# Kernel tuning notes

Hardware: AMD Instinct MI355X
Metric: run time of the kernel (lower is better)

Reference implementation:

```python
import jax, jax.numpy as jnp
import numpy as np

E, IN, H, OUT = 8, 512, 1024, 512   # num_experts, input_size, hidden_size, output_size
HH = H // 2                          # expert-MLP hidden (512)
GIN, GH = 5, E                       # gating GRU input / hidden


def gru_layer(x, w_ih, w_hh, b_ih, b_hh):
    """torch.nn.GRU single layer, batch_first. x: [B,T,I] -> ys: [B,T,Hd].
    Gate order in 3*Hd dims: reset, update, new."""
    Hd = w_hh.shape[1]
    def step(h, xt):
        gi = xt @ w_ih.T + b_ih          # [B,3Hd]
        gh = h @ w_hh.T + b_hh
        ir, iz, inn = jnp.split(gi, 3, axis=-1)
        hr, hz, hn = jnp.split(gh, 3, axis=-1)
        r = jax.nn.sigmoid(ir + hr)
        z = jax.nn.sigmoid(iz + hz)
        n = jnp.tanh(inn + r * hn)
        h = (1.0 - z) * n + z * h
        return h, h
    h0 = jnp.zeros((x.shape[0], Hd), x.dtype)
    _, ys = jax.lax.scan(step, h0, jnp.swapaxes(x, 0, 1))
    return jnp.swapaxes(ys, 0, 1)


def _uniform(key, shape, fan_in, fan_out):
    bound = np.sqrt(6.0 / (fan_in * fan_out))
    return jax.random.uniform(key, shape, jnp.float32, -bound, bound)


def setup_inputs() -> dict:
    key = jax.random.key(0)
    ks = jax.random.split(key, 16)
    g = 1.0 / np.sqrt(GH)
    m = 1.0 / np.sqrt(H)
    inp = {
        "X": jax.random.normal(ks[0], (128, 100, IN), jnp.float32),
        # gating GRU: 2 layers, input 5 -> hidden E
        "gw_ih0": jax.random.uniform(ks[1], (3 * GH, GIN), jnp.float32, -g, g),
        "gw_hh0": jax.random.uniform(ks[2], (3 * GH, GH), jnp.float32, -g, g),
        "gb_ih0": jnp.zeros((3 * GH,), jnp.float32),
        "gb_hh0": jnp.zeros((3 * GH,), jnp.float32),
        "gw_ih1": jax.random.uniform(ks[3], (3 * GH, GH), jnp.float32, -g, g),
        "gw_hh1": jax.random.uniform(ks[4], (3 * GH, GH), jnp.float32, -g, g),
        "gb_ih1": jnp.zeros((3 * GH,), jnp.float32),
        "gb_hh1": jnp.zeros((3 * GH,), jnp.float32),
        # main GRU: 1 layer, input IN -> hidden H
        "mw_ih": jax.random.uniform(ks[5], (3 * H, IN), jnp.float32, -m, m),
        "mw_hh": jax.random.uniform(ks[6], (3 * H, H), jnp.float32, -m, m),
        "mb_ih": jnp.zeros((3 * H,), jnp.float32),
        "mb_hh": jnp.zeros((3 * H,), jnp.float32),
        # expert MLP weights [E, in, out], biases [E, out]
        "w1": _uniform(ks[7], (E, H, HH), H, HH),
        "b1": jnp.zeros((E, HH), jnp.float32),
        "w2": _uniform(ks[8], (E, HH, HH), HH, HH),
        "b2": jnp.zeros((E, HH), jnp.float32),
        "w3": _uniform(ks[9], (E, HH, OUT), HH, OUT),
        "b3": jnp.zeros((E, OUT), jnp.float32),
    }
    return inp


def _moe_layer(x, coef, w, b):
    # same math as sum(x[...,None] * sum_e(coef_e * W_e), dim=1) + coef @ b
    return jnp.einsum("be,bi,eio->bo", coef, x, w) + coef @ b


def reference(X, gw_ih0, gw_hh0, gb_ih0, gb_hh0, gw_ih1, gw_hh1, gb_ih1, gb_hh1,
              mw_ih, mw_hh, mb_ih, mb_hh, w1, b1, w2, b2, w3, b3):
    Xg = X[:, :, -GIN:]
    h0 = gru_layer(Xg, gw_ih0, gw_hh0, gb_ih0, gb_hh0)
    h1 = gru_layer(h0, gw_ih1, gw_hh1, gb_ih1, gb_hh1)
    omega = jax.nn.softmax(h1[:, -1, :], axis=-1)          # [B,E]
    Z = gru_layer(X, mw_ih, mw_hh, mb_ih, mb_hh)[:, -1, :]  # [B,H]
    a1 = jax.nn.elu(_moe_layer(Z, omega, w1, b1))
    a2 = jax.nn.elu(_moe_layer(a1, omega, w2, b2))
    Y = _moe_layer(a2, omega, w3, b3)
    return jnp.clip(Y, 0.0, 1.0)
```

## Files before the change

kernel.cpp:

```cpp
#include <hip/hip_runtime.h>
#include <cmath>

#define B_   128
#define T_   100
#define IN_  512
#define H_   1024
#define E_   8
#define HH_  512
#define GIN_ 5
#define GH_  8

#define A_LO_  49152
#define BOFF_  98304
#define LDSZ2  147456
#define A_LOF 49152
#define BB_HI 98304
#define BB_LO 114688
#define LDSZF 131072

typedef unsigned long long u64t;
typedef unsigned int uint32;
typedef __attribute__((ext_vector_type(8))) short bf16x8;
typedef __attribute__((ext_vector_type(4))) float f32x4;

__device__ __forceinline__ float sigf(float x) { return 1.0f / (1.0f + expf(-x)); }

__device__ __forceinline__ float4 ld_h4_sc1(const float4* p) {
  const u64t* q = (const u64t*)p;
  u64t a = __hip_atomic_load(q,     __ATOMIC_RELAXED, __HIP_MEMORY_SCOPE_AGENT);
  u64t b = __hip_atomic_load(q + 1, __ATOMIC_RELAXED, __HIP_MEMORY_SCOPE_AGENT);
  union { u64t u; float2 f; } ca, cb;
  ca.u = a; cb.u = b;
  return make_float4(ca.f.x, ca.f.y, cb.f.x, cb.f.y);
}

__device__ __forceinline__ void st_u64_sc1(void* p, u64t v) {
  __hip_atomic_store((u64t*)p, v, __ATOMIC_RELAXED, __HIP_MEMORY_SCOPE_AGENT);
}

__device__ __forceinline__ void gridbar(unsigned* c) {
  __syncthreads();
  if (threadIdx.x == 0) {
    __hip_atomic_fetch_add(c, 1u, __ATOMIC_RELEASE, __HIP_MEMORY_SCOPE_AGENT);
    while (__hip_atomic_load(c, __ATOMIC_RELAXED, __HIP_MEMORY_SCOPE_AGENT) < gridDim.x) {
      __builtin_amdgcn_s_sleep(1);
    }
  }
  __syncthreads();
}

__device__ __forceinline__ uint32 bf16_rne(float f) {
  uint32 u = __builtin_bit_cast(uint32, f);
  return (u + 0x7FFFu + ((u >> 16) & 1u)) >> 16;
}

__device__ __forceinline__ void split2(float f0, float f1, uint32& h, uint32& l) {
  uint32 h0 = bf16_rne(f0), h1 = bf16_rne(f1);
  float hf0 = __builtin_bit_cast(float, h0 << 16);
  float hf1 = __builtin_bit_cast(float, h1 << 16);
  uint32 l0 = bf16_rne(f0 - hf0), l1 = bf16_rne(f1 - hf1);
  h = h0 | (h1 << 16);
  l = l0 | (l1 << 16);
}

__device__ __forceinline__ void gl_lds16(const char* g, char* l) {
  __builtin_amdgcn_global_load_lds(
      (const __attribute__((address_space(1))) uint32*)(const void*)g,
      (__attribute__((address_space(3))) uint32*)(void*)l, 16, 0, 0);
}

__global__ __launch_bounds__(256) void xsplit_kernel(
    const float* __restrict__ X, char* __restrict__ xpl)
{
  int idx = blockIdx.x * 256 + threadIdx.x;
  int lane = idx & 63;
  int n   = (idx >> 6) & 7;
  int KT  = (idx >> 9) & 15;
  int t   = idx >> 13;
  int b   = n * 16 + (lane & 15);
  int k   = KT * 32 + ((lane >> 4) << 3);
  const float* src = X + ((size_t)b * T_ + t) * IN_ + k;
  float4 va = *(const float4*)src;
  float4 vb = *(const float4*)(src + 4);
  uint32 h0,h1,h2,h3,l0,l1,l2,l3;
  split2(va.x, va.y, h0, l0); split2(va.z, va.w, h1, l1);
  split2(vb.x, vb.y, h2, l2); split2(vb.z, vb.w, h3, l3);
  size_t off = ((((size_t)t * 16 + KT) * 8 + n) << 10) + ((size_t)lane << 4);
  *(uint4*)(xpl + off)            = make_uint4(h0, h1, h2, h3);
  *(uint4*)(xpl + 13107200 + off) = make_uint4(l0, l1, l2, l3);
}

__global__ __launch_bounds__(1024, 4) void gru_mfma2(
    const char* __restrict__ xpl, char* __restrict__ ringp,
    const float* __restrict__ wih, const float* __restrict__ whh,
    const float* __restrict__ bih, const float* __restrict__ bhh,
    float* __restrict__ hq, unsigned* __restrict__ barr)
{
  extern __shared__ char lds[];
  const int tid  = threadIdx.x;
  const int lane = tid & 63;
  const int wv   = __builtin_amdgcn_readfirstlane(tid >> 6);
  const int nt   = wv & 7;
  const int ktw  = wv >> 3;
  const int j0   = blockIdx.x << 2;

  for (int ii = tid * 2; ii < 24576; ii += 2048) {
    int r = ii / 1536, k = ii - r * 1536;
    int jj = r & 3, g = r >> 2;
    float f0, f1;
    if (k < IN_) {
      if (g == 3) { f0 = 0.f; f1 = 0.f; }
      else {
        const float* p = wih + (size_t)(((g == 2 ? 2 : g) * H_) + j0 + jj) * IN_ + k;
        f0 = p[0]; f1 = p[1];
      }
    } else {
      if (g == 2) { f0 = 0.f; f1 = 0.f; }
      else {
        const float* p = whh + (size_t)(((g == 3 ? 2 : g) * H_) + j0 + jj) * H_ + (k - IN_);
        f0 = p[0]; f1 = p[1];
      }
    }
    uint32 h, l; split2(f0, f1, h, l);
    int KT = k >> 5, k32 = k & 31;
    int ln  = r + ((k32 >> 3) << 4);
    int off = (KT << 10) + (ln << 4) + ((k32 & 7) << 1);
    *(uint32*)(lds + off)         = h;
    *(uint32*)(lds + A_LO_ + off) = l;
  }

  const int ejj = tid >> 7, eb = tid & 127;
  float bir = 0.f, biz = 0.f, bin = 0.f, bhr = 0.f, bhz = 0.f, bhn = 0.f;
  if (tid < 512) {
    int j = j0 + ejj;
    bir = bih[j]; biz = bih[H_ + j]; bin = bih[2 * H_ + j];
    bhr = bhh[j]; bhz = bhh[H_ + j]; bhn = bhh[2 * H_ + j];
  }
  float hprev_r = 0.f;
  __syncthreads();

  const char* xsrc0 = xpl + (size_t)ktw * 13107200 + ((size_t)nt << 10) + ((size_t)lane << 4);
  const char* hsrc0 = ringp + (size_t)ktw * 262144 + ((size_t)nt << 10) + ((size_t)lane << 4);
  char* const tilebase = lds + BOFF_ + (((ktw << 3) + nt) << 10);

  const size_t pw_off = ((((size_t)(j0 >> 5)) * 8) << 10);

  for (int t = 0; t < T_; ++t) {
    const char* xs = xsrc0 + (size_t)t * 131072;
    const char* hs = hsrc0 + (size_t)t * 524288;
    f32x4 acc = {0.f, 0.f, 0.f, 0.f};

#define STAGE(cc) { const char* g = ((cc) < 16) ? (xs + (size_t)(cc) * 8192) \
                                                : (hs + (size_t)((cc) - 16) * 8192); \
                    gl_lds16(g, lds + BOFF_ + ((cc) % 3) * 16384 - BOFF_ + BOFF_ \
                             + (((ktw << 3) + nt) << 10) - (((ktw << 3) + nt) << 10) \
                             + ((cc) % 3) * 0); }
#undef STAGE

    gl_lds16(xs + 0 * 8192, tilebase + 0 * 16384);
    gl_lds16(xs + 1 * 8192, tilebase + 1 * 16384);

    #pragma unroll
    for (int c = 0; c < 48; ++c) {
      if (c < 46) {
        const int cn = c + 2;
        const char* g = (cn < 16) ? (xs + (size_t)cn * 8192)
                                  : (hs + (size_t)(cn - 16) * 8192);
        gl_lds16(g, tilebase + (cn % 3) * 16384);
        asm volatile("s_waitcnt vmcnt(2)" ::: "memory");
      } else if (c == 46) {
        asm volatile("s_waitcnt vmcnt(1)" ::: "memory");
      } else {
        asm volatile("s_waitcnt vmcnt(0)" ::: "memory");
      }
      __builtin_amdgcn_s_barrier();
      __builtin_amdgcn_sched_barrier(0);
      if (ktw == (c & 1)) {
        bf16x8 ah = *(const bf16x8*)(lds + (c << 10) + (lane << 4));
        bf16x8 al = *(const bf16x8*)(lds + A_LO_ + (c << 10) + (lane << 4));
        const char* bb = lds + BOFF_ + (c % 3) * 16384;
        bf16x8 bh = *(const bf16x8*)(bb + (nt << 10) + (lane << 4));
        bf16x8 bl = *(const bf16x8*)(bb + 8192 + (nt << 10) + (lane << 4));
        acc = __builtin_amdgcn_mfma_f32_16x16x32_bf16(ah, bh, acc, 0, 0, 0);
        acc = __builtin_amdgcn_mfma_f32_16x16x32_bf16(ah, bl, acc, 0, 0, 0);
        acc = __builtin_amdgcn_mfma_f32_16x16x32_bf16(al, bh, acc, 0, 0, 0);
      }
      __builtin_amdgcn_sched_barrier(0);
      __builtin_amdgcn_s_barrier();
    }

    *(f32x4*)(lds + BOFF_ + (((ktw << 3) + nt) << 10) + (lane << 4)) = acc;
    __syncthreads();

    if (tid < 512) {
      float sv[4];
      #pragma unroll
      for (int g = 0; g < 4; ++g) {
        int lr = (eb & 15) | (g << 4);
        const char* d0 = lds + BOFF_ + (((eb >> 4)) << 10) + (lr << 4) + (ejj << 2);
        float v0 = *(const float*)d0;
        float v1 = *(const float*)(d0 + 8192);
        sv[g] = v0 + v1;
      }
      float rr = sigf(sv[0] + bir + bhr);
      float zz = sigf(sv[1] + biz + bhz);
      float nn = tanhf(sv[2] + bin + rr * (sv[3] + bhn));
      float hv = (1.f - zz) * nn + zz * hprev_r;
      hprev_r = hv;
      ((float*)(lds + BOFF_ + 16384))[(ejj << 7) + eb] = hv;
      if (t == T_ - 1) hq[((blockIdx.x * 128 + eb) << 2) + ejj] = hv;
    }
    __syncthreads();

    if (tid < 128) {
      const int b = tid;
      const float* hl = (const float*)(lds + BOFF_ + 16384);
      uint32 hh[4], ll[4];
      #pragma unroll
      for (int i = 0; i < 4; ++i) {
        float v = hl[(i << 7) + b];
        uint32 hb = bf16_rne(v);
        float hf = __builtin_bit_cast(float, hb << 16);
        ll[i] = bf16_rne(v - hf);
        hh[i] = hb;
      }
      u64t HI = (u64t)hh[0] | ((u64t)hh[1] << 16) | ((u64t)hh[2] << 32) | ((u64t)hh[3] << 48);
      u64t LO = (u64t)ll[0] | ((u64t)ll[1] << 16) | ((u64t)ll[2] << 32) | ((u64t)ll[3] << 48);
      int lane_w = (((j0 & 31) >> 3) << 4) | (b & 15);
      size_t byteoff = pw_off + (((size_t)(b >> 4)) << 10) + ((size_t)lane_w << 4) + ((j0 & 4) ? 8 : 0);
      char* base = ringp + (size_t)(t + 1) * 524288;
      st_u64_sc1(base + byteoff, HI);
      st_u64_sc1(base + 262144 + byteoff, LO);
    }
    gridbar(barr + t);
  }
}

__device__ __forceinline__ int boff(int kt, int nt, int lane) {
  return (((((kt << 3) + nt) << 6) + lane) << 4) ^ ((nt & 3) << 5);
}

__global__ __launch_bounds__(256) void xt_kernel(
    const float* __restrict__ X, float4* __restrict__ XT4)
{
  int idx = blockIdx.x * 256 + threadIdx.x;
  int b  = idx & 127;
  int kq = (idx >> 7) & 127;
  int t  = idx >> 14;
  XT4[idx] = *(const float4*)(X + ((size_t)b * T_ + t) * IN_ + kq * 4);
}

template<bool RING>
__global__ __launch_bounds__(1024, 4) void gru_mfma(
    const float4* __restrict__ XT4, const float* __restrict__ X, int use_xt,
    const float* __restrict__ wih, const float* __restrict__ whh,
    const float* __restrict__ bih, const float* __restrict__ bhh,
    float* __restrict__ ring, unsigned* __restrict__ barr)
{
  extern __shared__ char lds[];
  const int tid  = threadIdx.x;
  const int lane = tid & 63;
  const int wv   = __builtin_amdgcn_readfirstlane(tid >> 6);
  const int nt   = wv & 7;
  const int ktw  = wv >> 3;
  const int j0   = blockIdx.x << 2;

  for (int ii = tid * 2; ii < 24576; ii += 2048) {
    int r = ii / 1536, k = ii - r * 1536;
    int jj = r & 3, g = r >> 2;
    float f0, f1;
    if (k < IN_) {
      if (g == 3) { f0 = 0.f; f1 = 0.f; }
      else {
        const float* p = wih + (size_t)(((g == 2 ? 2 : g) * H_) + j0 + jj) * IN_ + k;
        f0 = p[0]; f1 = p[1];
      }
    } else {
      if (g == 2) { f0 = 0.f; f1 = 0.f; }
      else {
        const float* p = whh + (size_t)(((g == 3 ? 2 : g) * H_) + j0 + jj) * H_ + (k - IN_);
        f0 = p[0]; f1 = p[1];
      }
    }
    uint32 h, l; split2(f0, f1, h, l);
    int KT = k >> 5, k32 = k & 31;
    int ln  = r + ((k32 >> 3) << 4);
    int off = (KT << 10) + (ln << 4) + ((k32 & 7) << 1);
    *(uint32*)(lds + off)         = h;
    *(uint32*)(lds + A_LOF + off) = l;
  }

  const int ejj = tid >> 7, eb = tid & 127;
  float bir = 0.f, biz = 0.f, bin = 0.f, bhr = 0.f, bhz = 0.f, bhn = 0.f;
  if (tid < 512) {
    int j = j0 + ejj;
    bir = bih[j]; biz = bih[H_ + j]; bin = bih[2 * H_ + j];
    bhr = bhh[j]; bhz = bhh[H_ + j]; bhn = bhh[2 * H_ + j];
  }
  __syncthreads();

  const int kq_loc = tid >> 7;
  const int sb     = tid & 127;
  const int s_nt   = sb >> 4;
  const int lane_w = (sb & 15) + ((kq_loc >> 1) << 4);
  const int sub8   = (kq_loc & 1) << 3;

  for (int t = 0; t < T_; ++t) {
    const float4* __restrict__ hp4 =
        (const float4*)ring + (size_t)(RING ? t : (t & 1)) * 32768;
    float* __restrict__ hnf =
        ring + (size_t)(RING ? (t + 1) : ((t + 1) & 1)) * 131072;
    const float4* __restrict__ xt_t = XT4 + (size_t)t * 16384;

    f32x4 acc = {0.f, 0.f, 0.f, 0.f};

    #pragma unroll 1
    for (int c = 0; c < 24; ++c) {
      #pragma unroll
      for (int i = 0; i < 2; ++i) {
        int kqg = (c << 4) + kq_loc + (i << 3);
        float4 v;
        if (kqg < 128) {
          if (use_xt) v = xt_t[kqg * 128 + sb];
          else        v = *(const float4*)(X + ((size_t)sb * T_ + t) * IN_ + (kqg << 2));
        } else {
          v = RING ? hp4[(kqg - 128) * 128 + sb]
                   : ld_h4_sc1(hp4 + (kqg - 128) * 128 + sb);
        }
        uint32 h01, h23, l01, l23;
        split2(v.x, v.y, h01, l01);
        split2(v.z, v.w, h23, l23);
        int bo = boff(i, s_nt, lane_w) + sub8;
        *(uint2*)(lds + BB_HI + bo) = make_uint2(h01, h23);
        *(uint2*)(lds + BB_LO + bo) = make_uint2(l01, l23);
      }
      __syncthreads();
      {
        int KT = (c << 1) + ktw;
        bf16x8 ah = *(const bf16x8*)(lds + (KT << 10) + (lane << 4));
        bf16x8 al = *(const bf16x8*)(lds + A_LOF + (KT << 10) + (lane << 4));
        int bo = boff(ktw, nt, lane);
        bf16x8 bh = *(const bf16x8*)(lds + BB_HI + bo);
        bf16x8 bl = *(const bf16x8*)(lds + BB_LO + bo);
        acc = __builtin_amdgcn_mfma_f32_16x16x32_bf16(ah, bh, acc, 0, 0, 0);
        acc = __builtin_amdgcn_mfma_f32_16x16x32_bf16(ah, bl, acc, 0, 0, 0);
        acc = __builtin_amdgcn_mfma_f32_16x16x32_bf16(al, bh, acc, 0, 0, 0);
      }
      __syncthreads();
    }

    *(f32x4*)(lds + BB_HI + boff(ktw, nt, lane)) = acc;
    __syncthreads();
    if (tid < 512) {
      float sv[4];
      #pragma unroll
      for (int g = 0; g < 4; ++g) {
        int r  = (g << 2) + ejj;
        int lr = (eb & 15) + ((r >> 2) << 4);
        int rg = (r & 3) << 2;
        float v0 = *(const float*)(lds + BB_HI + boff(0, eb >> 4, lr) + rg);
        float v1 = *(const float*)(lds + BB_HI + boff(1, eb >> 4, lr) + rg);
        sv[g] = v0 + v1;
      }
      float rr = sigf(sv[0] + bir + bhr);
      float zz = sigf(sv[1] + biz + bhz);
      float nn = tanhf(sv[2] + bin + rr * (sv[3] + bhn));
      int hidx = ((blockIdx.x * 128 + eb) << 2) + ejj;
      float hpv;
      if (RING) hpv = ((const float*)hp4)[hidx];
      else      hpv = __hip_atomic_load(&((const float*)hp4)[hidx],
                                        __ATOMIC_RELAXED, __HIP_MEMORY_SCOPE_AGENT);
      float hv = (1.f - zz) * nn + zz * hpv;
      __hip_atomic_store(&hnf[hidx], hv, __ATOMIC_RELAXED, __HIP_MEMORY_SCOPE_AGENT);
    }
    gridbar(barr + t);
  }
}

__global__ __launch_bounds__(256) void hfin_kernel(
    const float* __restrict__ h4, float* __restrict__ out)
{
  int idx = blockIdx.x * 256 + threadIdx.x;
  int b = idx >> 10, k = idx & 1023;
  out[idx] = h4[(((k >> 2) * 128 + b) << 2) + (k & 3)];
}

__global__ __launch_bounds__(64, 1) void gating_kernel(
    const float* __restrict__ X,
    const float* __restrict__ gwih0, const float* __restrict__ gwhh0,
    const float* __restrict__ gbih0, const float* __restrict__ gbhh0,
    const float* __restrict__ gwih1, const float* __restrict__ gwhh1,
    const float* __restrict__ gbih1, const float* __restrict__ gbhh1,
    float* __restrict__ omega)
{
  const int b = blockIdx.x;
  const int g = threadIdx.x;
  const int u = g & 7;
  float wi0[GIN_] = {}, wh0[GH_] = {}, wi1[GH_] = {}, wh1[GH_] = {};
  float bi0 = 0.f, bh0 = 0.f, bi1 = 0.f, bh1 = 0.f;
  if (g < 3 * GH_) {
    #pragma unroll
    for (int i = 0; i < GIN_; ++i) wi0[i] = gwih0[g * GIN_ + i];
    #pragma unroll
    for (int k = 0; k < GH_; ++k) { wh0[k] = gwhh0[g * GH_ + k]; wi1[k] = gwih1[g * GH_ + k]; wh1[k] = gwhh1[g * GH_ + k]; }
    bi0 = gbih0[g]; bh0 = gbhh0[g]; bi1 = gbih1[g]; bh1 = gbhh1[g];
  }
  float h0[GH_] = {}, h1[GH_] = {};
  for (int t = 0; t < T_; ++t) {
    float xt[GIN_];
    #pragma unroll
    for (int i = 0; i < GIN_; ++i) xt[i] = X[((size_t)b * T_ + t) * IN_ + (IN_ - GIN_) + i];
    float px = bi0, ph = bh0;
    #pragma unroll
    for (int i = 0; i < GIN_; ++i) px = fmaf(xt[i], wi0[i], px);
    #pragma unroll
    for (int k = 0; k < GH_; ++k) ph = fmaf(h0[k], wh0[k], ph);
    float s = px + ph;
    float s_r = __shfl(s, u);
    float s_z = __shfl(s, 8 + u);
    float nval = tanhf(px + sigf(s_r) * ph);
    float zval = sigf(s_z);
    float hnew = (1.f - zval) * nval + zval * h0[u];
    #pragma unroll
    for (int k = 0; k < GH_; ++k) h0[k] = __shfl(hnew, 16 + k);
    float px1 = bi1, ph1 = bh1;
    #pragma unroll
    for (int k = 0; k < GH_; ++k) px1 = fmaf(h0[k], wi1[k], px1);
    #pragma unroll
    for (int k = 0; k < GH_; ++k) ph1 = fmaf(h1[k], wh1[k], ph1);
    float s1 = px1 + ph1;
    float s1r = __shfl(s1, u);
    float s1z = __shfl(s1, 8 + u);
    float n1 = tanhf(px1 + sigf(s1r) * ph1);
    float z1 = sigf(s1z);
    float h1new = (1.f - z1) * n1 + z1 * h1[u];
    #pragma unroll
    for (int k = 0; k < GH_; ++k) h1[k] = __shfl(h1new, 16 + k);
  }
  if (g < GH_) {
    float m = h1[0];
    #pragma unroll
    for (int k = 1; k < GH_; ++k) m = fmaxf(m, h1[k]);
    float sum = 0.f;
    #pragma unroll
    for (int k = 0; k < GH_; ++k) sum += expf(h1[k] - m);
    omega[b * GH_ + g] = expf(h1[g] - m) / sum;
  }
}

__global__ __launch_bounds__(256, 2) void moe_kernel(
    const float* __restrict__ in, const float* __restrict__ w,
    const float* __restrict__ bias, const float* __restrict__ omega,
    float* __restrict__ out, int K, int act)
{
  __shared__ float4 lin4[64 * 32];
  __shared__ float  ldsw[E_ * 4 * 128];
  const int tid  = threadIdx.x;
  const int bh   = blockIdx.x & 1;
  const int jt   = blockIdx.x >> 1;
  const int wv   = tid >> 6;
  const int lane = tid & 63;
  const int j0   = jt * 4;
  const int j    = __builtin_amdgcn_readfirstlane(j0 + wv);
  const int b    = bh * 64 + lane;

  float acc[E_] = {0.f,0.f,0.f,0.f,0.f,0.f,0.f,0.f};
  const float4* row4 = &lin4[lane * 32];
  const int nch = K / 128;

  for (int c = 0; c < nch; ++c) {
    __syncthreads();
    const int k0 = c * 128;
    #pragma unroll
    for (int it = 0; it < 8; ++it) {
      int f = it * 256 + tid;
      int bb = f >> 5, q = f & 31;
      float4 v = *(const float4*)(in + (size_t)(bh * 64 + bb) * K + k0 + q * 4);
      lin4[bb * 32 + ((q & 24) | ((q ^ bb) & 7))] = v;
    }
    #pragma unroll
    for (int it = 0; it < 4; ++it) {
      int f = it * 256 + tid;
      int e = f >> 7, k = f & 127;
      float4 v = *(const float4*)(w + ((size_t)e * K + k0 + k) * HH_ + j0);
      ldsw[(e * 4 + 0) * 128 + k] = v.x;
      ldsw[(e * 4 + 1) * 128 + k] = v.y;
      ldsw[(e * 4 + 2) * 128 + k] = v.z;
      ldsw[(e * 4 + 3) * 128 + k] = v.w;
    }
    __syncthreads();
    #pragma unroll 2
    for (int q = 0; q < 32; ++q) {
      float4 xv = row4[(q & 24) | ((q ^ lane) & 7)];
      #pragma unroll
      for (int e = 0; e < E_; ++e) {
        const float4 wq = *(const float4*)&ldsw[(e * 4 + wv) * 128 + 4 * q];
        acc[e] = fmaf(xv.x, wq.x, acc[e]);
        acc[e] = fmaf(xv.y, wq.y, acc[e]);
        acc[e] = fmaf(xv.z, wq.z, acc[e]);
        acc[e] = fmaf(xv.w, wq.w, acc[e]);
      }
    }
  }

  float om[E_];
  #pragma unroll
  for (int e = 0; e < E_; ++e) om[e] = omega[b * E_ + e];
  float v = 0.f;
  #pragma unroll
  for (int e = 0; e < E_; ++e) v = fmaf(om[e], acc[e] + bias[e * HH_ + j], v);
  if (act == 0) v = (v > 0.f) ? v : expm1f(v);
  else          v = fminf(fmaxf(v, 0.f), 1.f);
  out[(size_t)b * HH_ + j] = v;
}

extern "C" void kernel_launch(void* const* d_in, const int* in_sizes, int n_in,
                              void* d_out, int out_size, void* d_ws, size_t ws_size,
                              hipStream_t stream) {
  (void)in_sizes; (void)n_in; (void)out_size;
  const float* X     = (const float*)d_in[0];
  const float* gwih0 = (const float*)d_in[1];
  const float* gwhh0 = (const float*)d_in[2];
  const float* gbih0 = (const float*)d_in[3];
  const float* gbhh0 = (const float*)d_in[4];
  const float* gwih1 = (const float*)d_in[5];
  const float* gwhh1 = (const float*)d_in[6];
  const float* gbih1 = (const float*)d_in[7];
  const float* gbhh1 = (const float*)d_in[8];
  const float* mwih  = (const float*)d_in[9];
  const float* mwhh  = (const float*)d_in[10];
  const float* mbih  = (const float*)d_in[11];
  const float* mbhh  = (const float*)d_in[12];
  const float* w1    = (const float*)d_in[13];
  const float* b1    = (const float*)d_in[14];
  const float* w2    = (const float*)d_in[15];
  const float* b2    = (const float*)d_in[16];
  const float* w3    = (const float*)d_in[17];
  const float* b3    = (const float*)d_in[18];

  const size_t HBUF = (size_t)B_ * H_;
  size_t tierS_f = 256 + HBUF + 101 * HBUF + 1024 + 2 * (size_t)B_ * HH_ + HBUF + 6553600;
  const size_t XTF = (size_t)T_ * IN_ * B_;
  size_t ringA = 256 + (size_t)(T_ + 1) * HBUF + HBUF + 1024 + 2 * (size_t)B_ * HH_ + XTF;
  size_t ringB = 256 + 2 * HBUF + HBUF + 1024 + 2 * (size_t)B_ * HH_ + XTF;

  float* ws = (float*)d_ws;

  if (ws_size >= tierS_f * sizeof(float)) {
    unsigned* barr = (unsigned*)ws;
    float* hq    = ws + 256;
    float* ringp = hq + HBUF;
    float* om    = ringp + 101 * HBUF;
    float* a1    = om + 1024;
    float* a2    = a1 + (size_t)B_ * HH_;
    float* hfin  = a2 + (size_t)B_ * HH_;
    float* xpl   = hfin + HBUF;

    (void)hipMemsetAsync(d_ws, 0, 256 * sizeof(float), stream);
    (void)hipMemsetAsync(ringp, 0, 524288, stream);
    (void)hipFuncSetAttribute((const void*)gru_mfma2,
                        hipFuncAttributeMaxDynamicSharedMemorySize, LDSZ2);

    gating_kernel<<<128, 64, 0, stream>>>(X, gwih0, gwhh0, gbih0, gbhh0,
                                          gwih1, gwhh1, gbih1, gbhh1, om);
    xsplit_kernel<<<3200, 256, 0, stream>>>(X, (char*)xpl);
    gru_mfma2<<<256, 1024, LDSZ2, stream>>>((const char*)xpl, (char*)ringp,
        mwih, mwhh, mbih, mbhh, hq, barr);
    hfin_kernel<<<512, 256, 0, stream>>>(hq, hfin);
    moe_kernel<<<256, 256, 0, stream>>>(hfin, w1, b1, om, a1, H_, 0);
    moe_kernel<<<256, 256, 0, stream>>>(a1, w2, b2, om, a2, HH_, 0);
    moe_kernel<<<256, 256, 0, stream>>>(a2, w3, b3, om, (float*)d_out, HH_, 1);
    return;
  }

  int tierA   = ws_size >= ringA * sizeof(float);
  int use_xt  = tierA || (ws_size >= ringB * sizeof(float));
  int R       = tierA ? (T_ + 1) : 2;

  unsigned* barr = (unsigned*)ws;
  float* ring = ws + 256;
  float* hfin = ring + (size_t)R * HBUF;
  float* om   = hfin + HBUF;
  float* a1   = om + 1024;
  float* a2   = a1 + (size_t)B_ * HH_;
  float* XT   = a2 + (size_t)B_ * HH_;

  (void)hipMemsetAsync(d_ws, 0, (256 + HBUF) * sizeof(float), stream);
  (void)hipFuncSetAttribute((const void*)gru_mfma<true>,
                      hipFuncAttributeMaxDynamicSharedMemorySize, LDSZF);
  (void)hipFuncSetAttribute((const void*)gru_mfma<false>,
                      hipFuncAttributeMaxDynamicSharedMemorySize, LDSZF);

  gating_kernel<<<128, 64, 0, stream>>>(X, gwih0, gwhh0, gbih0, gbhh0,
                                        gwih1, gwhh1, gbih1, gbhh1, om);
  if (use_xt)
    xt_kernel<<<(T_ * 128 * 128) / 256, 256, 0, stream>>>(X, (float4*)XT);

  if (tierA)
    gru_mfma<true><<<256, 1024, LDSZF, stream>>>((const float4*)XT, X, use_xt,
        mwih, mwhh, mbih, mbhh, ring, barr);
  else
    gru_mfma<false><<<256, 1024, LDSZF, stream>>>((const float4*)XT, X, use_xt,
        mwih, mwhh, mbih, mbhh, ring, barr);

  const float* hlast = ring + (size_t)(tierA ? T_ : (T_ & 1)) * HBUF;
  hfin_kernel<<<512, 256, 0, stream>>>(hlast, hfin);
  moe_kernel<<<256, 256, 0, stream>>>(hfin, w1, b1, om, a1, H_, 0);
  moe_kernel<<<256, 256, 0, stream>>>(a1, w2, b2, om, a2, HH_, 0);
  moe_kernel<<<256, 256, 0, stream>>>(a2, w3, b3, om, (float*)d_out, HH_, 1);
}
```

Before: 1.758 ms.

## Restructure GRU MFMA loop: paired K-chunks, register-held weights, cross-step prefetch

The persistent GRU kernel now computes two K-chunks per iteration, one per half of the waves, instead of leaving half the waves idle each chunk. This halves the number of barrier-separated iterations. The last 8 K-chunks of the recurrent weights are held in registers, which frees LDS for a double-buffered B staging area. The first x-chunk of the next timestep is prefetched before the step's reduction. The aim is to cut per-step barrier count and serial latency in the latency-bound recurrence, at the cost of more registers and more complex indexing under a 1024-thread, 4-wave-per-SIMD launch bound.

```diff
diff --git a/kernel.cpp b/kernel.cpp
--- a/kernel.cpp
+++ b/kernel.cpp
@@ -10,9 +10,10 @@
 #define GIN_ 5
 #define GH_  8
 
-#define A_LO_  49152
-#define BOFF_  98304
-#define LDSZ2  147456
+#define A_LO_  40960
+#define BOFF_  81920
+#define BOFF2_ 114688
+#define LDSZ4  147456
 #define A_LOF 49152
 #define BB_HI 98304
 #define BB_LO 114688
@@ -90,7 +91,27 @@
   *(uint4*)(xpl + 13107200 + off) = make_uint4(l0, l1, l2, l3);
 }
 
-__global__ __launch_bounds__(1024, 4) void gru_mfma2(
+__device__ __forceinline__ void stage_pair(
+    char* lds, const char* xpl, const char* ringp,
+    int q, int tx, int th, int sp, int spl, int snp, int lane)
+{
+  const int cc = 2 * q + sp;
+  char* dst0 = lds + BOFF_ + ((q & 1) << 15) + (sp << 14) + (spl << 13);
+  #pragma unroll
+  for (int i = 0; i < 2; ++i) {
+    const int nt = (snp << 1) + i;
+    const char* src;
+    if (cc < 16)
+      src = xpl + (size_t)spl * 13107200
+          + ((((size_t)tx * 16 + cc) * 8 + nt) << 10) + ((size_t)lane << 4);
+    else
+      src = ringp + (size_t)th * 524288 + ((size_t)spl << 18)
+          + ((size_t)((cc - 16) * 8 + nt) << 10) + ((size_t)lane << 4);
+    gl_lds16(src, dst0 + (nt << 10));
+  }
+}
+
+__global__ __launch_bounds__(1024, 4) void gru_mfma4(
     const char* __restrict__ xpl, char* __restrict__ ringp,
     const float* __restrict__ wih, const float* __restrict__ whh,
     const float* __restrict__ bih, const float* __restrict__ bhh,
@@ -100,12 +121,15 @@
   const int tid  = threadIdx.x;
   const int lane = tid & 63;
   const int wv   = __builtin_amdgcn_readfirstlane(tid >> 6);
-  const int nt   = wv & 7;
-  const int ktw  = wv >> 3;
+  const int cw   = wv >> 3;
+  const int ntc  = wv & 7;
+  const int sp   = wv & 1;
+  const int spl  = (wv >> 1) & 1;
+  const int snp  = wv >> 2;
   const int j0   = blockIdx.x << 2;
 
-  for (int ii = tid * 2; ii < 24576; ii += 2048) {
-    int r = ii / 1536, k = ii - r * 1536;
+  for (int ii = tid * 2; ii < 20480; ii += 2048) {
+    int r = ii / 1280, k = ii - r * 1280;
     int jj = r & 3, g = r >> 2;
     float f0, f1;
     if (k < IN_) {
@@ -129,6 +153,33 @@
     *(uint32*)(lds + A_LO_ + off) = l;
   }
 
+  bf16x8 rah[4], ral[4];
+  {
+    const int rr = lane & 15, k8 = lane >> 4;
+    const int jj = rr & 3, g = rr >> 2;
+    #pragma unroll
+    for (int i = 0; i < 4; ++i) {
+      const int KT = 40 + 2 * i + cw;
+      const int kh = KT * 32 + k8 * 8 - IN_;
+      bf16x8 hv, lv;
+      if (g == 2) {
+        #pragma unroll
+        for (int e = 0; e < 8; ++e) { hv[e] = 0; lv[e] = 0; }
+      } else {
+        const float* p = whh + (size_t)(((g == 3 ? 2 : g) * H_) + j0 + jj) * H_ + kh;
+        #pragma unroll
+        for (int e = 0; e < 8; ++e) {
+          float v = p[e];
+          uint32 hb = bf16_rne(v);
+          float hf = __builtin_bit_cast(float, hb << 16);
+          uint32 lb = bf16_rne(v - hf);
+          hv[e] = (short)hb; lv[e] = (short)lb;
+        }
+      }
+      rah[i] = hv; ral[i] = lv;
+    }
+  }
+
   const int ejj = tid >> 7, eb = tid & 127;
   float bir = 0.f, biz = 0.f, bin = 0.f, bhr = 0.f, bhz = 0.f, bhn = 0.f;
   if (tid < 512) {
@@ -137,50 +188,27 @@
     bhr = bhh[j]; bhz = bhh[H_ + j]; bhn = bhh[2 * H_ + j];
   }
   float hprev_r = 0.f;
+  const size_t pw_off = ((((size_t)(j0 >> 5)) * 8) << 10);
   __syncthreads();
 
-  const char* xsrc0 = xpl + (size_t)ktw * 13107200 + ((size_t)nt << 10) + ((size_t)lane << 4);
-  const char* hsrc0 = ringp + (size_t)ktw * 262144 + ((size_t)nt << 10) + ((size_t)lane << 4);
-  char* const tilebase = lds + BOFF_ + (((ktw << 3) + nt) << 10);
-
-  const size_t pw_off = ((((size_t)(j0 >> 5)) * 8) << 10);
+  stage_pair(lds, xpl, ringp, 0, 0, 0, sp, spl, snp, lane);
 
   for (int t = 0; t < T_; ++t) {
-    const char* xs = xsrc0 + (size_t)t * 131072;
-    const char* hs = hsrc0 + (size_t)t * 524288;
     f32x4 acc = {0.f, 0.f, 0.f, 0.f};
 
-#define STAGE(cc) { const char* g = ((cc) < 16) ? (xs + (size_t)(cc) * 8192) \
-                                                : (hs + (size_t)((cc) - 16) * 8192); \
-                    gl_lds16(g, lds + BOFF_ + ((cc) % 3) * 16384 - BOFF_ + BOFF_ \
-                             + (((ktw << 3) + nt) << 10) - (((ktw << 3) + nt) << 10) \
-                             + ((cc) % 3) * 0); }
-#undef STAGE
-
-    gl_lds16(xs + 0 * 8192, tilebase + 0 * 16384);
-    gl_lds16(xs + 1 * 8192, tilebase + 1 * 16384);
-
-    #pragma unroll
-    for (int c = 0; c < 48; ++c) {
-      if (c < 46) {
-        const int cn = c + 2;
-        const char* g = (cn < 16) ? (xs + (size_t)cn * 8192)
-                                  : (hs + (size_t)(cn - 16) * 8192);
-        gl_lds16(g, tilebase + (cn % 3) * 16384);
-        asm volatile("s_waitcnt vmcnt(2)" ::: "memory");
-      } else if (c == 46) {
-        asm volatile("s_waitcnt vmcnt(1)" ::: "memory");
-      } else {
-        asm volatile("s_waitcnt vmcnt(0)" ::: "memory");
-      }
+    #pragma unroll 4
+    for (int p = 0; p < 20; ++p) {
+      stage_pair(lds, xpl, ringp, p + 1, t, t, sp, spl, snp, lane);
+      asm volatile("s_waitcnt vmcnt(2)" ::: "memory");
       __builtin_amdgcn_s_barrier();
       __builtin_amdgcn_sched_barrier(0);
-      if (ktw == (c & 1)) {
+      {
+        const int c = 2 * p + cw;
         bf16x8 ah = *(const bf16x8*)(lds + (c << 10) + (lane << 4));
         bf16x8 al = *(const bf16x8*)(lds + A_LO_ + (c << 10) + (lane << 4));
-        const char* bb = lds + BOFF_ + (c % 3) * 16384;
-        bf16x8 bh = *(const bf16x8*)(bb + (nt << 10) + (lane << 4));
-        bf16x8 bl = *(const bf16x8*)(bb + 8192 + (nt << 10) + (lane << 4));
+        const char* bb = lds + BOFF_ + ((p & 1) << 15) + (cw << 14);
+        bf16x8 bh = *(const bf16x8*)(bb + (ntc << 10) + (lane << 4));
+        bf16x8 bl = *(const bf16x8*)(bb + 8192 + (ntc << 10) + (lane << 4));
         acc = __builtin_amdgcn_mfma_f32_16x16x32_bf16(ah, bh, acc, 0, 0, 0);
         acc = __builtin_amdgcn_mfma_f32_16x16x32_bf16(ah, bl, acc, 0, 0, 0);
         acc = __builtin_amdgcn_mfma_f32_16x16x32_bf16(al, bh, acc, 0, 0, 0);
@@ -189,7 +217,33 @@
       __builtin_amdgcn_s_barrier();
     }
 
-    *(f32x4*)(lds + BOFF_ + (((ktw << 3) + nt) << 10) + (lane << 4)) = acc;
+    #pragma unroll
+    for (int i = 0; i < 4; ++i) {
+      const int p = 20 + i;
+      if (p < 23) {
+        stage_pair(lds, xpl, ringp, p + 1, t, t, sp, spl, snp, lane);
+        asm volatile("s_waitcnt vmcnt(2)" ::: "memory");
+      } else if (t < T_ - 1) {
+        stage_pair(lds, xpl, ringp, 0, t + 1, t + 1, sp, spl, snp, lane);
+        asm volatile("s_waitcnt vmcnt(2)" ::: "memory");
+      } else {
+        asm volatile("s_waitcnt vmcnt(0)" ::: "memory");
+      }
+      __builtin_amdgcn_s_barrier();
+      __builtin_amdgcn_sched_barrier(0);
+      {
+        const char* bb = lds + BOFF_ + ((p & 1) << 15) + (cw << 14);
+        bf16x8 bh = *(const bf16x8*)(bb + (ntc << 10) + (lane << 4));
+        bf16x8 bl = *(const bf16x8*)(bb + 8192 + (ntc << 10) + (lane << 4));
+        acc = __builtin_amdgcn_mfma_f32_16x16x32_bf16(rah[i], bh, acc, 0, 0, 0);
+        acc = __builtin_amdgcn_mfma_f32_16x16x32_bf16(rah[i], bl, acc, 0, 0, 0);
+        acc = __builtin_amdgcn_mfma_f32_16x16x32_bf16(ral[i], bh, acc, 0, 0, 0);
+      }
+      __builtin_amdgcn_sched_barrier(0);
+      __builtin_amdgcn_s_barrier();
+    }
+
+    *(f32x4*)(lds + BOFF2_ + (((cw << 3) + ntc) << 10) + (lane << 4)) = acc;
     __syncthreads();
 
     if (tid < 512) {
@@ -197,7 +251,7 @@
       #pragma unroll
       for (int g = 0; g < 4; ++g) {
         int lr = (eb & 15) | (g << 4);
-        const char* d0 = lds + BOFF_ + (((eb >> 4)) << 10) + (lr << 4) + (ejj << 2);
+        const char* d0 = lds + BOFF2_ + (((eb >> 4)) << 10) + (lr << 4) + (ejj << 2);
         float v0 = *(const float*)d0;
         float v1 = *(const float*)(d0 + 8192);
         sv[g] = v0 + v1;
@@ -207,14 +261,14 @@
       float nn = tanhf(sv[2] + bin + rr * (sv[3] + bhn));
       float hv = (1.f - zz) * nn + zz * hprev_r;
       hprev_r = hv;
-      ((float*)(lds + BOFF_ + 16384))[(ejj << 7) + eb] = hv;
+      ((float*)(lds + BOFF2_ + 16384))[(ejj << 7) + eb] = hv;
       if (t == T_ - 1) hq[((blockIdx.x * 128 + eb) << 2) + ejj] = hv;
     }
     __syncthreads();
 
     if (tid < 128) {
       const int b = tid;
-      const float* hl = (const float*)(lds + BOFF_ + 16384);
+      const float* hl = (const float*)(lds + BOFF2_ + 16384);
       uint32 hh[4], ll[4];
       #pragma unroll
       for (int i = 0; i < 4; ++i) {
@@ -558,13 +612,13 @@
 
     (void)hipMemsetAsync(d_ws, 0, 256 * sizeof(float), stream);
     (void)hipMemsetAsync(ringp, 0, 524288, stream);
-    (void)hipFuncSetAttribute((const void*)gru_mfma2,
-                        hipFuncAttributeMaxDynamicSharedMemorySize, LDSZ2);
+    (void)hipFuncSetAttribute((const void*)gru_mfma4,
+                        hipFuncAttributeMaxDynamicSharedMemorySize, LDSZ4);
 
     gating_kernel<<<128, 64, 0, stream>>>(X, gwih0, gwhh0, gbih0, gbhh0,
                                           gwih1, gwhh1, gbih1, gbhh1, om);
     xsplit_kernel<<<3200, 256, 0, stream>>>(X, (char*)xpl);
-    gru_mfma2<<<256, 1024, LDSZ2, stream>>>((const char*)xpl, (char*)ringp,
+    gru_mfma4<<<256, 1024, LDSZ4, stream>>>((const char*)xpl, (char*)ringp,
         mwih, mwhh, mbih, mbhh, hq, barr);
     hfin_kernel<<<512, 256, 0, stream>>>(hq, hfin);
     moe_kernel<<<256, 256, 0, stream>>>(hfin, w1, b1, om, a1, H_, 0);
```

New measurement: 1.758 ms. No clear change (-0.0%).

## Restructure persistent GRU kernel around 32x32 MFMA with register-resident weights

Applied to the files above, without the earlier changes.

The persistent GRU recurrence kernel is rebuilt so each block owns 8 hidden units across half the batch and uses 32x32x16 bf16 MFMAs. The high half of the split weights lives in registers and the low half mostly in LDS, with K split across 8 wave groups and partial sums reduced through LDS in two phases. The X and hidden-state ring layouts change to match the new tiles. The final hidden state is written directly in [B,H] order, so the separate hfin transpose kernel is dropped. This aims to cut per-step LDS traffic and MFMA issue count on the serial timestep loop, at the cost of much higher register pressure and an extra barrier-separated reduction phase.

```diff
diff --git a/kernel.cpp b/kernel.cpp
--- a/kernel.cpp
+++ b/kernel.cpp
@@ -10,9 +10,11 @@
 #define GIN_ 5
 #define GH_  8
 
-#define A_LO_  49152
-#define BOFF_  98304
-#define LDSZ2  147456
+#define ALO_   0
+#define BOFF_  81920
+#define DUMP_  114688
+#define HL_    81920
+#define LDSZ5  147456
 #define A_LOF 49152
 #define BB_HI 98304
 #define BB_LO 114688
@@ -20,8 +22,9 @@
 
 typedef unsigned long long u64t;
 typedef unsigned int uint32;
-typedef __attribute__((ext_vector_type(8))) short bf16x8;
-typedef __attribute__((ext_vector_type(4))) float f32x4;
+typedef __attribute__((ext_vector_type(8)))  short bf16x8;
+typedef __attribute__((ext_vector_type(4)))  float f32x4;
+typedef __attribute__((ext_vector_type(16))) float f32x16;
 
 __device__ __forceinline__ float sigf(float x) { return 1.0f / (1.0f + expf(-x)); }
 
@@ -72,25 +75,46 @@
 __global__ __launch_bounds__(256) void xsplit_kernel(
     const float* __restrict__ X, char* __restrict__ xpl)
 {
-  int idx = blockIdx.x * 256 + threadIdx.x;
+  int idx  = blockIdx.x * 256 + threadIdx.x;
   int lane = idx & 63;
-  int n   = (idx >> 6) & 7;
-  int KT  = (idx >> 9) & 15;
-  int t   = idx >> 13;
-  int b   = n * 16 + (lane & 15);
-  int k   = KT * 32 + ((lane >> 4) << 3);
+  int bq   = (idx >> 6) & 3;
+  int KT   = (idx >> 8) & 31;
+  int t    = idx >> 13;
+  int col  = lane & 31, kg = lane >> 5;
+  int b    = bq * 32 + col;
+  int k    = KT * 16 + kg * 8;
   const float* src = X + ((size_t)b * T_ + t) * IN_ + k;
   float4 va = *(const float4*)src;
   float4 vb = *(const float4*)(src + 4);
   uint32 h0,h1,h2,h3,l0,l1,l2,l3;
   split2(va.x, va.y, h0, l0); split2(va.z, va.w, h1, l1);
   split2(vb.x, vb.y, h2, l2); split2(vb.z, vb.w, h3, l3);
-  size_t off = ((((size_t)t * 16 + KT) * 8 + n) << 10) + ((size_t)lane << 4);
+  size_t off = ((((size_t)t * 32 + KT) * 4 + bq) << 10) + ((size_t)lane << 4);
   *(uint4*)(xpl + off)            = make_uint4(h0, h1, h2, h3);
   *(uint4*)(xpl + 13107200 + off) = make_uint4(l0, l1, l2, l3);
 }
 
-__global__ __launch_bounds__(1024, 4) void gru_mfma2(
+__device__ __forceinline__ void stageS(
+    char* lds, const char* xpl, const char* ringp,
+    int t, int pn, int ko, int nt, int bq, int lane)
+{
+  const int KT = 8 * pn + ko;
+  char* dst = lds + BOFF_ + ((pn & 1) << 15) + (ko << 12) + (nt << 11);
+  const char *s0, *s1;
+  if (KT < 32) {
+    size_t o = ((((size_t)t * 32 + KT) * 4 + bq) << 10) + ((size_t)lane << 4);
+    s0 = xpl + o;
+    s1 = xpl + 13107200 + o;
+  } else {
+    size_t o = (size_t)t * 524288 + ((((size_t)(KT - 32) * 4) + bq) << 10) + ((size_t)lane << 4);
+    s0 = ringp + o;
+    s1 = ringp + 262144 + o;
+  }
+  gl_lds16(s0, dst);
+  gl_lds16(s1, dst + 1024);
+}
+
+__global__ __launch_bounds__(1024, 4) void gru_mfma5(
     const char* __restrict__ xpl, char* __restrict__ ringp,
     const float* __restrict__ wih, const float* __restrict__ whh,
     const float* __restrict__ bih, const float* __restrict__ bhh,
@@ -100,137 +124,164 @@
   const int tid  = threadIdx.x;
   const int lane = tid & 63;
   const int wv   = __builtin_amdgcn_readfirstlane(tid >> 6);
-  const int nt   = wv & 7;
-  const int ktw  = wv >> 3;
-  const int j0   = blockIdx.x << 2;
-
-  for (int ii = tid * 2; ii < 24576; ii += 2048) {
-    int r = ii / 1536, k = ii - r * 1536;
-    int jj = r & 3, g = r >> 2;
-    float f0, f1;
-    if (k < IN_) {
-      if (g == 3) { f0 = 0.f; f1 = 0.f; }
-      else {
-        const float* p = wih + (size_t)(((g == 2 ? 2 : g) * H_) + j0 + jj) * IN_ + k;
-        f0 = p[0]; f1 = p[1];
-      }
-    } else {
-      if (g == 2) { f0 = 0.f; f1 = 0.f; }
-      else {
-        const float* p = whh + (size_t)(((g == 3 ? 2 : g) * H_) + j0 + jj) * H_ + (k - IN_);
-        f0 = p[0]; f1 = p[1];
-      }
-    }
-    uint32 h, l; split2(f0, f1, h, l);
-    int KT = k >> 5, k32 = k & 31;
-    int ln  = r + ((k32 >> 3) << 4);
-    int off = (KT << 10) + (ln << 4) + ((k32 & 7) << 1);
-    *(uint32*)(lds + off)         = h;
-    *(uint32*)(lds + A_LO_ + off) = l;
-  }
-
-  const int ejj = tid >> 7, eb = tid & 127;
+  const int q    = wv >> 1;
+  const int ntc  = wv & 1;
+  const int bid  = blockIdx.x;
+  const int j0   = (bid >> 1) << 3;
+  const int bhalf = bid & 1;
+  const int bq   = bhalf * 2 + ntc;
+
+  bf16x8 rah[12], ral2[2];
+  {
+    const int rrow = lane & 31, g = rrow >> 3, jl_a = rrow & 7, kg_a = lane >> 5;
+    const int jA = j0 + jl_a;
+    #pragma unroll
+    for (int p = 0; p < 12; ++p) {
+      const int KT = 8 * p + q;
+      const int kb = KT * 16 + kg_a * 8;
+      bf16x8 hi8, lo8;
+      bool zero = (p <= 3) ? (g == 3) : (g == 2);
+      if (zero) {
+        #pragma unroll
+        for (int e = 0; e < 8; ++e) { hi8[e] = 0; lo8[e] = 0; }
+      } else {
+        const float* srcp;
+        if (p <= 3) srcp = wih + (size_t)(g * H_ + jA) * IN_ + kb;
+        else        srcp = whh + (size_t)(((g == 3) ? 2 : g) * H_ + jA) * H_ + (kb - IN_);
+        float4 va = *(const float4*)srcp;
+        float4 vb = *(const float4*)(srcp + 4);
+        float vv[8] = {va.x, va.y, va.z, va.w, vb.x, vb.y, vb.z, vb.w};
+        #pragma unroll
+        for (int e = 0; e < 8; ++e) {
+          uint32 hb = bf16_rne(vv[e]);
+          float hf = __builtin_bit_cast(float, hb << 16);
+          uint32 lb = bf16_rne(vv[e] - hf);
+          hi8[e] = (short)hb; lo8[e] = (short)lb;
+        }
+      }
+      rah[p] = hi8;
+      if (p <= 9) {
+        if (ntc == 0)
+          *(bf16x8*)(lds + ALO_ + (KT << 10) + (lane << 4)) = lo8;
+      } else {
+        ral2[p - 10] = lo8;
+      }
+    }
+  }
+
+  const int ejl = tid >> 6, eb = tid & 63;
   float bir = 0.f, biz = 0.f, bin = 0.f, bhr = 0.f, bhz = 0.f, bhn = 0.f;
   if (tid < 512) {
-    int j = j0 + ejj;
+    int j = j0 + ejl;
     bir = bih[j]; biz = bih[H_ + j]; bin = bih[2 * H_ + j];
     bhr = bhh[j]; bhz = bhh[H_ + j]; bhn = bhh[2 * H_ + j];
   }
   float hprev_r = 0.f;
   __syncthreads();
 
-  const char* xsrc0 = xpl + (size_t)ktw * 13107200 + ((size_t)nt << 10) + ((size_t)lane << 4);
-  const char* hsrc0 = ringp + (size_t)ktw * 262144 + ((size_t)nt << 10) + ((size_t)lane << 4);
-  char* const tilebase = lds + BOFF_ + (((ktw << 3) + nt) << 10);
-
-  const size_t pw_off = ((((size_t)(j0 >> 5)) * 8) << 10);
-
   for (int t = 0; t < T_; ++t) {
-    const char* xs = xsrc0 + (size_t)t * 131072;
-    const char* hs = hsrc0 + (size_t)t * 524288;
-    f32x4 acc = {0.f, 0.f, 0.f, 0.f};
-
-#define STAGE(cc) { const char* g = ((cc) < 16) ? (xs + (size_t)(cc) * 8192) \
-                                                : (hs + (size_t)((cc) - 16) * 8192); \
-                    gl_lds16(g, lds + BOFF_ + ((cc) % 3) * 16384 - BOFF_ + BOFF_ \
-                             + (((ktw << 3) + nt) << 10) - (((ktw << 3) + nt) << 10) \
-                             + ((cc) % 3) * 0); }
-#undef STAGE
-
-    gl_lds16(xs + 0 * 8192, tilebase + 0 * 16384);
-    gl_lds16(xs + 1 * 8192, tilebase + 1 * 16384);
-
-    #pragma unroll
-    for (int c = 0; c < 48; ++c) {
-      if (c < 46) {
-        const int cn = c + 2;
-        const char* g = (cn < 16) ? (xs + (size_t)cn * 8192)
-                                  : (hs + (size_t)(cn - 16) * 8192);
-        gl_lds16(g, tilebase + (cn % 3) * 16384);
+    f32x16 acc = {0.f,0.f,0.f,0.f,0.f,0.f,0.f,0.f,0.f,0.f,0.f,0.f,0.f,0.f,0.f,0.f};
+
+    stageS(lds, xpl, ringp, t, 0, q, ntc, bq, lane);
+
+    #pragma unroll
+    for (int p = 0; p < 12; ++p) {
+      if (p < 11) {
+        stageS(lds, xpl, ringp, t, p + 1, q, ntc, bq, lane);
         asm volatile("s_waitcnt vmcnt(2)" ::: "memory");
-      } else if (c == 46) {
-        asm volatile("s_waitcnt vmcnt(1)" ::: "memory");
       } else {
         asm volatile("s_waitcnt vmcnt(0)" ::: "memory");
       }
       __builtin_amdgcn_s_barrier();
       __builtin_amdgcn_sched_barrier(0);
-      if (ktw == (c & 1)) {
-        bf16x8 ah = *(const bf16x8*)(lds + (c << 10) + (lane << 4));
-        bf16x8 al = *(const bf16x8*)(lds + A_LO_ + (c << 10) + (lane << 4));
-        const char* bb = lds + BOFF_ + (c % 3) * 16384;
-        bf16x8 bh = *(const bf16x8*)(bb + (nt << 10) + (lane << 4));
-        bf16x8 bl = *(const bf16x8*)(bb + 8192 + (nt << 10) + (lane << 4));
-        acc = __builtin_amdgcn_mfma_f32_16x16x32_bf16(ah, bh, acc, 0, 0, 0);
-        acc = __builtin_amdgcn_mfma_f32_16x16x32_bf16(ah, bl, acc, 0, 0, 0);
-        acc = __builtin_amdgcn_mfma_f32_16x16x32_bf16(al, bh, acc, 0, 0, 0);
+      {
+        const int KT = 8 * p + q;
+        bf16x8 al;
+        if (p < 10) al = *(const bf16x8*)(lds + ALO_ + (KT << 10) + (lane << 4));
+        else        al = ral2[p - 10];
+        const char* bbp = lds + BOFF_ + ((p & 1) << 15) + (q << 12) + (ntc << 11);
+        bf16x8 bh = *(const bf16x8*)(bbp + (lane << 4));
+        bf16x8 bl = *(const bf16x8*)(bbp + 1024 + (lane << 4));
+        acc = __builtin_amdgcn_mfma_f32_32x32x16_bf16(rah[p], bh, acc, 0, 0, 0);
+        acc = __builtin_amdgcn_mfma_f32_32x32x16_bf16(rah[p], bl, acc, 0, 0, 0);
+        acc = __builtin_amdgcn_mfma_f32_32x32x16_bf16(al,     bh, acc, 0, 0, 0);
       }
       __builtin_amdgcn_sched_barrier(0);
       __builtin_amdgcn_s_barrier();
     }
 
-    *(f32x4*)(lds + BOFF_ + (((ktw << 3) + nt) << 10) + (lane << 4)) = acc;
+    float sv[4] = {0.f, 0.f, 0.f, 0.f};
+    const int bb5 = eb >> 5, bl_ = eb & 31, jlh = ejl >> 2, jli = ejl & 3;
+    const int laneoff = ((bl_ + (jlh << 5)) << 4) + (jli << 2);
+
+    if (q < 4) {
+      char* d = lds + DUMP_ + ((q & 3) << 13) + (ntc << 12) + (lane << 4);
+      *(f32x4*)(d)          = (f32x4){acc[0],  acc[1],  acc[2],  acc[3]};
+      *(f32x4*)(d + 1024)   = (f32x4){acc[4],  acc[5],  acc[6],  acc[7]};
+      *(f32x4*)(d + 2048)   = (f32x4){acc[8],  acc[9],  acc[10], acc[11]};
+      *(f32x4*)(d + 3072)   = (f32x4){acc[12], acc[13], acc[14], acc[15]};
+    }
     __syncthreads();
-
     if (tid < 512) {
-      float sv[4];
       #pragma unroll
-      for (int g = 0; g < 4; ++g) {
-        int lr = (eb & 15) | (g << 4);
-        const char* d0 = lds + BOFF_ + (((eb >> 4)) << 10) + (lr << 4) + (ejj << 2);
-        float v0 = *(const float*)d0;
-        float v1 = *(const float*)(d0 + 8192);
-        sv[g] = v0 + v1;
+      for (int qq = 0; qq < 4; ++qq) {
+        const char* base = lds + DUMP_ + (qq << 13) + (bb5 << 12);
+        #pragma unroll
+        for (int g = 0; g < 4; ++g) sv[g] += *(const float*)(base + (g << 10) + laneoff);
+      }
+    }
+    __syncthreads();
+    if (q >= 4) {
+      char* d = lds + DUMP_ + ((q & 3) << 13) + (ntc << 12) + (lane << 4);
+      *(f32x4*)(d)          = (f32x4){acc[0],  acc[1],  acc[2],  acc[3]};
+      *(f32x4*)(d + 1024)   = (f32x4){acc[4],  acc[5],  acc[6],  acc[7]};
+      *(f32x4*)(d + 2048)   = (f32x4){acc[8],  acc[9],  acc[10], acc[11]};
+      *(f32x4*)(d + 3072)   = (f32x4){acc[12], acc[13], acc[14], acc[15]};
+    }
+    __syncthreads();
+    if (tid < 512) {
+      #pragma unroll
+      for (int qq = 0; qq < 4; ++qq) {
+        const char* base = lds + DUMP_ + (qq << 13) + (bb5 << 12);
+        #pragma unroll
+        for (int g = 0; g < 4; ++g) sv[g] += *(const float*)(base + (g << 10) + laneoff);
       }
       float rr = sigf(sv[0] + bir + bhr);
       float zz = sigf(sv[1] + biz + bhz);
       float nn = tanhf(sv[2] + bin + rr * (sv[3] + bhn));
       float hv = (1.f - zz) * nn + zz * hprev_r;
       hprev_r = hv;
-      ((float*)(lds + BOFF_ + 16384))[(ejj << 7) + eb] = hv;
-      if (t == T_ - 1) hq[((blockIdx.x * 128 + eb) << 2) + ejj] = hv;
+      ((float*)(lds + HL_))[(ejl << 6) + eb] = hv;
+      if (t == T_ - 1) hq[(size_t)(bhalf * 64 + eb) * H_ + (j0 + ejl)] = hv;
     }
     __syncthreads();
 
-    if (tid < 128) {
+    if (tid < 64) {
       const int b = tid;
-      const float* hl = (const float*)(lds + BOFF_ + 16384);
-      uint32 hh[4], ll[4];
+      const float* hl = (const float*)(lds + HL_);
+      uint32 hi16[8], lo16[8];
       #pragma unroll
-      for (int i = 0; i < 4; ++i) {
-        float v = hl[(i << 7) + b];
+      for (int jl = 0; jl < 8; ++jl) {
+        float v = hl[(jl << 6) + b];
         uint32 hb = bf16_rne(v);
         float hf = __builtin_bit_cast(float, hb << 16);
-        ll[i] = bf16_rne(v - hf);
-        hh[i] = hb;
-      }
-      u64t HI = (u64t)hh[0] | ((u64t)hh[1] << 16) | ((u64t)hh[2] << 32) | ((u64t)hh[3] << 48);
-      u64t LO = (u64t)ll[0] | ((u64t)ll[1] << 16) | ((u64t)ll[2] << 32) | ((u64t)ll[3] << 48);
-      int lane_w = (((j0 & 31) >> 3) << 4) | (b & 15);
-      size_t byteoff = pw_off + (((size_t)(b >> 4)) << 10) + ((size_t)lane_w << 4) + ((j0 & 4) ? 8 : 0);
-      char* base = ringp + (size_t)(t + 1) * 524288;
-      st_u64_sc1(base + byteoff, HI);
-      st_u64_sc1(base + 262144 + byteoff, LO);
+        lo16[jl] = bf16_rne(v - hf);
+        hi16[jl] = hb;
+      }
+      u64t H0 = (u64t)hi16[0] | ((u64t)hi16[1] << 16) | ((u64t)hi16[2] << 32) | ((u64t)hi16[3] << 48);
+      u64t H1 = (u64t)hi16[4] | ((u64t)hi16[5] << 16) | ((u64t)hi16[6] << 32) | ((u64t)hi16[7] << 48);
+      u64t L0 = (u64t)lo16[0] | ((u64t)lo16[1] << 16) | ((u64t)lo16[2] << 32) | ((u64t)lo16[3] << 48);
+      u64t L1 = (u64t)lo16[4] | ((u64t)lo16[5] << 16) | ((u64t)lo16[6] << 32) | ((u64t)lo16[7] << 48);
+      const int kg  = (bid >> 1) & 1;
+      const int KTh = bid >> 2;
+      const int bq2 = bhalf * 2 + (b >> 5);
+      const int lane_f = (b & 31) + (kg << 5);
+      size_t off = ((((size_t)KTh << 2) + bq2) << 10) + ((size_t)lane_f << 4);
+      char* basep = ringp + (size_t)(t + 1) * 524288;
+      st_u64_sc1(basep + off, H0);
+      st_u64_sc1(basep + off + 8, H1);
+      st_u64_sc1(basep + 262144 + off, L0);
+      st_u64_sc1(basep + 262144 + off + 8, L1);
     }
     gridbar(barr + t);
   }
@@ -474,9 +525,9 @@
     #pragma unroll
     for (int it = 0; it < 8; ++it) {
       int f = it * 256 + tid;
-      int bb = f >> 5, q = f & 31;
-      float4 v = *(const float4*)(in + (size_t)(bh * 64 + bb) * K + k0 + q * 4);
-      lin4[bb * 32 + ((q & 24) | ((q ^ bb) & 7))] = v;
+      int bb = f >> 5, qq = f & 31;
+      float4 v = *(const float4*)(in + (size_t)(bh * 64 + bb) * K + k0 + qq * 4);
+      lin4[bb * 32 + ((qq & 24) | ((qq ^ bb) & 7))] = v;
     }
     #pragma unroll
     for (int it = 0; it < 4; ++it) {
@@ -490,11 +541,11 @@
     }
     __syncthreads();
     #pragma unroll 2
-    for (int q = 0; q < 32; ++q) {
-      float4 xv = row4[(q & 24) | ((q ^ lane) & 7)];
+    for (int qq = 0; qq < 32; ++qq) {
+      float4 xv = row4[(qq & 24) | ((qq ^ lane) & 7)];
       #pragma unroll
       for (int e = 0; e < E_; ++e) {
-        const float4 wq = *(const float4*)&ldsw[(e * 4 + wv) * 128 + 4 * q];
+        const float4 wq = *(const float4*)&ldsw[(e * 4 + wv) * 128 + 4 * qq];
         acc[e] = fmaf(xv.x, wq.x, acc[e]);
         acc[e] = fmaf(xv.y, wq.y, acc[e]);
         acc[e] = fmaf(xv.z, wq.z, acc[e]);
@@ -553,21 +604,19 @@
     float* om    = ringp + 101 * HBUF;
     float* a1    = om + 1024;
     float* a2    = a1 + (size_t)B_ * HH_;
-    float* hfin  = a2 + (size_t)B_ * HH_;
-    float* xpl   = hfin + HBUF;
+    float* xpl   = a2 + (size_t)B_ * HH_ + HBUF;
 
     (void)hipMemsetAsync(d_ws, 0, 256 * sizeof(float), stream);
     (void)hipMemsetAsync(ringp, 0, 524288, stream);
-    (void)hipFuncSetAttribute((const void*)gru_mfma2,
-                        hipFuncAttributeMaxDynamicSharedMemorySize, LDSZ2);
+    (void)hipFuncSetAttribute((const void*)gru_mfma5,
+                        hipFuncAttributeMaxDynamicSharedMemorySize, LDSZ5);
 
     gating_kernel<<<128, 64, 0, stream>>>(X, gwih0, gwhh0, gbih0, gbhh0,
                                           gwih1, gwhh1, gbih1, gbhh1, om);
     xsplit_kernel<<<3200, 256, 0, stream>>>(X, (char*)xpl);
-    gru_mfma2<<<256, 1024, LDSZ2, stream>>>((const char*)xpl, (char*)ringp,
+    gru_mfma5<<<256, 1024, LDSZ5, stream>>>((const char*)xpl, (char*)ringp,
         mwih, mwhh, mbih, mbhh, hq, barr);
-    hfin_kernel<<<512, 256, 0, stream>>>(hq, hfin);
-    moe_kernel<<<256, 256, 0, stream>>>(hfin, w1, b1, om, a1, H_, 0);
+    moe_kernel<<<256, 256, 0, stream>>>(hq, w1, b1, om, a1, H_, 0);
     moe_kernel<<<256, 256, 0, stream>>>(a1, w2, b2, om, a2, HH_, 0);
     moe_kernel<<<256, 256, 0, stream>>>(a2, w3, b3, om, (float*)d_out, HH_, 1);
     return;
```

Result: faster. 1.537 ms (-12.6%).
